# Optimization experiments

Measured on AMD Instinct MI355X. Metric: run time of the kernel, lower is better.

## Reference

```python
import jax, jax.numpy as jnp
import numpy as np

N = 50000      # nodes
D = 16         # fixed in-degree per node
E = N * D      # edges
C = 128        # in_channels == hidden_channels
H = 128        # hidden_channels
ED = 16        # edge_dim
OUT = 2        # out_channels


def setup_inputs() -> dict:
    key = jax.random.key(0)
    ks = jax.random.split(key, 16)
    s = 0.05
    x = jax.random.normal(ks[0], (N, C), jnp.float32)
    src = jax.random.randint(ks[1], (E,), 0, N)
    dst = jnp.repeat(jnp.arange(N), D)           # sorted by destination, degree D each
    edge_index = jnp.stack([src, dst]).astype(jnp.int32)
    edge_attr = jax.random.normal(ks[2], (E, ED), jnp.float32)
    # 3 SAGEConv layers, each: LSTM(C->C) aggregator + lin_l(C->H, bias) + lin_r(C->H, no bias)
    Wih = jax.random.normal(ks[3], (3, 4 * C, C), jnp.float32) * s
    Whh = jax.random.normal(ks[4], (3, 4 * C, C), jnp.float32) * s
    bih = jax.random.normal(ks[5], (3, 4 * C), jnp.float32) * s
    bhh = jax.random.normal(ks[6], (3, 4 * C), jnp.float32) * s
    lin_l_W = jax.random.normal(ks[7], (3, H, C), jnp.float32) * s
    lin_l_b = jax.random.normal(ks[8], (3, H), jnp.float32) * s
    lin_r_W = jax.random.normal(ks[9], (3, H, C), jnp.float32) * s
    # edge MLP: (2H+ED)->H->H//2->OUT
    W1 = jax.random.normal(ks[10], (H, 2 * H + ED), jnp.float32) * s
    b1 = jax.random.normal(ks[11], (H,), jnp.float32) * s
    W2 = jax.random.normal(ks[12], (H // 2, H), jnp.float32) * s
    b2 = jax.random.normal(ks[13], (H // 2,), jnp.float32) * s
    W3 = jax.random.normal(ks[14], (OUT, H // 2), jnp.float32) * s
    b3 = jax.random.normal(ks[15], (OUT,), jnp.float32) * s
    return dict(x=x, edge_index=edge_index, edge_attr=edge_attr,
                Wih=Wih, Whh=Whh, bih=bih, bhh=bhh,
                lin_l_W=lin_l_W, lin_l_b=lin_l_b, lin_r_W=lin_r_W,
                W1=W1, b1=b1, W2=W2, b2=b2, W3=W3, b3=b3)


def _lstm_last(seq, wih, whh, bi, bh):
    # seq: [N, D, C] -> last LSTM output [N, C] (torch gate order i,f,g,o)
    h0 = jnp.zeros((seq.shape[0], whh.shape[1]), seq.dtype)

    def step(carry, xt):
        h, c = carry
        gates = xt @ wih.T + bi + h @ whh.T + bh
        i, f, g, o = jnp.split(gates, 4, axis=-1)
        c = jax.nn.sigmoid(f) * c + jax.nn.sigmoid(i) * jnp.tanh(g)
        h = jax.nn.sigmoid(o) * jnp.tanh(c)
        return (h, c), None

    (h, _), _ = jax.lax.scan(step, (h0, h0), seq.transpose(1, 0, 2))
    return h


def _sage_lstm(x, src, wih, whh, bi, bh, wl, bl, wr):
    # fixed degree D, edges sorted by dst -> group-by-dst is a reshape
    seq = x[src].reshape(N, D, -1)           # [N, D, C] neighbor sequences
    agg = _lstm_last(seq, wih, whh, bi, bh)  # [N, C]
    return agg @ wl.T + bl + x @ wr.T        # lin_l(agg) + lin_r(x)


def reference(x, edge_index, edge_attr, Wih, Whh, bih, bhh,
              lin_l_W, lin_l_b, lin_r_W, W1, b1, W2, b2, W3, b3):
    src, dst = edge_index[0], edge_index[1]
    h = x
    for l in range(3):
        h = jax.nn.relu(_sage_lstm(h, src, Wih[l], Whh[l], bih[l], bhh[l],
                                   lin_l_W[l], lin_l_b[l], lin_r_W[l]))
    # gather-concat edge MLP (dropout is identity in eval)
    feat = jnp.concatenate([h[src], h[dst], edge_attr], axis=1)  # [E, 2H+ED]
    e = jax.nn.relu(feat @ W1.T + b1)
    e = jax.nn.relu(e @ W2.T + b2)
    return e @ W3.T + b3
```

## Files before the change

### kernel.cpp

```cpp
#include <hip/hip_runtime.h>
#include <hip/hip_bf16.h>

#define NN 50000
#define DEG 16

typedef __attribute__((ext_vector_type(8))) short bfrag;
typedef __attribute__((ext_vector_type(4))) float f32x4;

__device__ __forceinline__ float bf2f(unsigned int u){ return __uint_as_float(u<<16); }
__device__ __forceinline__ unsigned short f2bf(float x){
  unsigned int u = __float_as_uint(x);
  unsigned int r = (u + 0x7fffu + ((u>>16)&1u)) >> 16;
  return (unsigned short)r;
}
__device__ __forceinline__ float fast_rcp(float x){ return __builtin_amdgcn_rcpf(x); }
__device__ __forceinline__ float sigmoidf_(float x){ return fast_rcp(1.f + __expf(-x)); }
__device__ __forceinline__ float tanh_fast(float x){
  float e = __expf(-2.f*fabsf(x));
  float r = (1.f - e)*fast_rcp(1.f + e);
  return copysignf(r, x);
}

#define SWZ(row) (((((row) ^ ((row)>>3)) & 7)) << 4)
#define SW4(row) (((row) & 15) << 4)

#define GLDS16(g, l) __builtin_amdgcn_global_load_lds( \
    (const __attribute__((address_space(1))) unsigned int*)(g), \
    (__attribute__((address_space(3))) unsigned int*)(l), 16, 0, 0)

__global__ void k_cvt(const float* __restrict__ in, unsigned short* __restrict__ out, int n){
  int i = blockIdx.x*256 + threadIdx.x;
  if (i < n) out[i] = f2bf(in[i]);
}

__global__ void k_prep_all(const float* __restrict__ Wih, const float* __restrict__ Whh,
                           const float* __restrict__ bih, const float* __restrict__ bhh,
                           const float* __restrict__ WlL, const float* __restrict__ WrL,
                           const float* __restrict__ W1,  const float* __restrict__ W2,
                           const float* __restrict__ W3,
                           unsigned short* __restrict__ Wcat, float* __restrict__ bsum,
                           unsigned short* __restrict__ Wlb,  unsigned short* __restrict__ Wrb,
                           unsigned short* __restrict__ W1nb,
                           unsigned short* __restrict__ W1eh, unsigned short* __restrict__ W1el,
                           unsigned short* __restrict__ W2h,  unsigned short* __restrict__ W2l,
                           unsigned short* __restrict__ W3p)
{
  int i = blockIdx.x*256 + threadIdx.x;
  if (i < 393216){
    int l = i >> 17;
    int rem = i & 131071;
    int row = rem >> 8, col = rem & 255;
    float v = (col < 128) ? Wih[((size_t)l*512 + row)*128 + col]
                          : Whh[((size_t)l*512 + row)*128 + (col-128)];
    Wcat[i] = f2bf(v);
  } else if (i < 394752){
    int k = i - 393216;
    bsum[k] = bih[k] + bhh[k];
  } else if (i < 443904){
    int k = i - 394752;
    Wlb[k] = f2bf(WlL[k]);
  } else if (i < 493056){
    int k = i - 443904;
    Wrb[k] = f2bf(WrL[k]);
  } else if (i < 509440){
    int k = i - 493056; int r = k >> 7, c = k & 127;
    W1nb[k] = f2bf(W1[(size_t)r*272 + c]);
  } else if (i < 525824){
    int k = i - 509440; int r = k >> 7, c = k & 127;
    W1nb[16384 + k] = f2bf(W1[(size_t)r*272 + 128 + c]);
  } else if (i < 534016){
    int k = i - 525824;
    float v = W2[k];
    unsigned short hi = f2bf(v);
    W2h[k] = hi; W2l[k] = f2bf(v - bf2f(hi));
  } else if (i < 536064){
    int k = i - 534016; int j = k >> 4, kk = k & 15;
    float v = W1[(size_t)j*272 + 256 + kk];
    unsigned short hi = f2bf(v);
    W1eh[k] = hi; W1el[k] = f2bf(v - bf2f(hi));
  } else if (i < 537088){
    int k = i - 536064; int nr = k >> 6, c = k & 63;
    W3p[k] = f2bf(nr < 2 ? W3[nr*64 + c] : 0.f);
  }
}

__global__ __launch_bounds__(256,4) void k_bgemm(
    const unsigned short* __restrict__ Ab, const unsigned short* __restrict__ A2b,
    const unsigned short* __restrict__ Wb, const unsigned short* __restrict__ W2b,
    const float* __restrict__ bias, const float* __restrict__ bias2,
    float* __restrict__ outF, unsigned short* __restrict__ outB,
    int ostride, int dorelu, int n)
{
  const int t  = threadIdx.x;
  const int w  = t >> 6;
  const int l  = t & 63;
  const int ln = l & 15, q = l >> 4;
  const int n0 = blockIdx.x*64;
  const int j0 = blockIdx.y*128 + w*32;

  int nodeM[4];
#pragma unroll
  for (int mt=0;mt<4;mt++){ int nd = n0 + mt*16 + ln; nodeM[mt] = nd < n ? nd : n-1; }

  f32x4 acc[4][2];
#pragma unroll
  for (int mt=0;mt<4;mt++)
#pragma unroll
    for (int nt=0;nt<2;nt++) acc[mt][nt] = (f32x4){0.f,0.f,0.f,0.f};

  auto pass = [&](const unsigned short* __restrict__ Ap, const unsigned short* __restrict__ Wp){
#pragma unroll
    for (int ks=0;ks<4;ks++){
      bfrag Af[4], Bf[2];
#pragma unroll
      for (int mt=0;mt<4;mt++)
        Af[mt] = *(const bfrag*)(Ap + (size_t)nodeM[mt]*128 + ks*32 + q*8);
#pragma unroll
      for (int nt=0;nt<2;nt++)
        Bf[nt] = *(const bfrag*)(Wp + (size_t)(j0 + nt*16 + ln)*128 + ks*32 + q*8);
#pragma unroll
      for (int mt=0;mt<4;mt++)
#pragma unroll
        for (int nt=0;nt<2;nt++)
          acc[mt][nt] = __builtin_amdgcn_mfma_f32_16x16x32_bf16(Af[mt], Bf[nt], acc[mt][nt], 0,0,0);
    }
  };
  pass(Ab, Wb);
  if (A2b) pass(A2b, W2b);

#pragma unroll
  for (int nt=0;nt<2;nt++){
    int j = j0 + nt*16 + ln;
    float bv = bias ? bias[j] : 0.f;
    if (bias2) bv += bias2[j];
#pragma unroll
    for (int mt=0;mt<4;mt++)
#pragma unroll
      for (int r=0;r<4;r++){
        int row = n0 + mt*16 + q*4 + r;
        if (row < n){
          float v = acc[mt][nt][r] + bv;
          if (dorelu) v = fmaxf(v, 0.f);
          if (outF) outF[(size_t)row*ostride + j] = v;
          if (outB) outB[(size_t)row*ostride + j] = f2bf(v);
        }
      }
  }
}

__global__ __launch_bounds__(512,2) void k_lstm9(
    const unsigned short* __restrict__ xin,
    const int* __restrict__ src,
    const unsigned short* __restrict__ Wcat,
    const float* __restrict__ bsum,
    const unsigned short* __restrict__ Wlb,
    const unsigned short* __restrict__ Wrb,
    const float* __restrict__ bl,
    unsigned short* __restrict__ hout,
    int n)
{
  __shared__ unsigned short hs[64*128];
  __shared__ unsigned short xbuf[2][64*128];
  __shared__ int srcs[64*16];
  const int t  = threadIdx.x;
  const int w  = t >> 6;
  const int l  = t & 63;
  const int ln = l & 15;
  const int q  = l >> 4;
  const int n0 = blockIdx.x * 64;

  for (int i = t; i < 1024; i += 512){
    int nl = i >> 4, st = i & 15;
    srcs[i] = (n0+nl < n) ? src[(size_t)(n0+nl)*16 + st] : 0;
  }

  bfrag A[4][8];
#pragma unroll
  for (int T=0;T<4;T++)
#pragma unroll
    for (int ks=0;ks<8;ks++)
      A[T][ks] = *(const bfrag*)(Wcat + (size_t)(T*128 + w*16 + ln)*256 + ks*32 + q*8);

  f32x4 bsv[4];
#pragma unroll
  for (int T=0;T<4;T++)
    bsv[T] = *(const f32x4*)(bsum + T*128 + w*16 + q*4);

  float c[4][4];
#pragma unroll
  for (int nt=0;nt<4;nt++)
#pragma unroll
    for (int r=0;r<4;r++) c[nt][r]=0.f;

  __syncthreads();

  auto stageX = [&](int step, int buf){
#pragma unroll
    for (int j=0;j<2;j++){
      int row  = w*8 + j*4 + (l>>4);
      int node = srcs[row*16 + step];
      const char* gsrc = (const char*)xin + (size_t)node*256 + (((l&15)*16) ^ SW4(row));
      char* ldst = (char*)&xbuf[buf][0] + (w*8 + j*4)*256;
      GLDS16(gsrc, ldst);
    }
  };

  stageX(0, 0);
  asm volatile("s_waitcnt vmcnt(0)" ::: "memory");
  __syncthreads();

  for (int step=0; step<16; step++){
    const int cur = step & 1;
    if (step < 15) stageX(step+1, cur^1);

#pragma unroll
    for (int p=0;p<2;p++){
      f32x4 acc[4][2];
#pragma unroll
      for (int T=0;T<4;T++)
#pragma unroll
        for (int ntl=0;ntl<2;ntl++) acc[T][ntl] = (f32x4){0.f,0.f,0.f,0.f};

#pragma unroll
      for (int ntl=0; ntl<2; ntl++){
        int node = p*32 + ntl*16 + ln;
        int swz  = SW4(node);
#pragma unroll
        for (int ks=0;ks<4;ks++){
          bfrag Bk = *(const bfrag*)((const char*)&xbuf[cur][0] + node*256 +
                       ((ks*64 + q*16) ^ swz));
#pragma unroll
          for (int T=0;T<4;T++)
            acc[T][ntl] = __builtin_amdgcn_mfma_f32_16x16x32_bf16(A[T][ks], Bk, acc[T][ntl], 0,0,0);
        }
        if (step > 0){
#pragma unroll
          for (int ks=4;ks<8;ks++){
            bfrag Bk = *(const bfrag*)((const char*)hs + node*256 +
                         (((ks-4)*64 + q*16) ^ swz));
#pragma unroll
            for (int T=0;T<4;T++)
              acc[T][ntl] = __builtin_amdgcn_mfma_f32_16x16x32_bf16(A[T][ks], Bk, acc[T][ntl], 0,0,0);
          }
        }
      }

      if (p == 1){
        asm volatile("s_waitcnt vmcnt(0)" ::: "memory");
      }
      __syncthreads();

#pragma unroll
      for (int ntl=0; ntl<2; ntl++){
        int nt = p*2 + ntl;
        int node = p*32 + ntl*16 + ln;
        float h[4];
#pragma unroll
        for (int r=0;r<4;r++){
          float iv = acc[0][ntl][r] + bsv[0][r];
          float fv = acc[1][ntl][r] + bsv[1][r];
          float gg = acc[2][ntl][r] + bsv[2][r];
          float ov = acc[3][ntl][r] + bsv[3][r];
          float cn = sigmoidf_(fv)*c[nt][r] + sigmoidf_(iv)*tanh_fast(gg);
          c[nt][r] = cn;
          h[r] = sigmoidf_(ov)*tanh_fast(cn);
        }
        unsigned pk01, pk23;
        asm("v_cvt_pk_bf16_f32 %0, %1, %2" : "=v"(pk01) : "v"(h[0]), "v"(h[1]));
        asm("v_cvt_pk_bf16_f32 %0, %1, %2" : "=v"(pk23) : "v"(h[2]), "v"(h[3]));
        uint2 pv; pv.x = pk01; pv.y = pk23;
        *(uint2*)((char*)hs + node*256 + (((w*32 + q*8)) ^ SW4(node))) = pv;
      }
    }
  }

  __syncthreads();
  {
    bfrag Al[4], Ar[4];
#pragma unroll
    for (int ks=0;ks<4;ks++){
      Al[ks] = *(const bfrag*)(Wlb + (size_t)(w*16+ln)*128 + ks*32 + q*8);
      Ar[ks] = *(const bfrag*)(Wrb + (size_t)(w*16+ln)*128 + ks*32 + q*8);
    }
    f32x4 blv = *(const f32x4*)(bl + w*16 + q*4);
#pragma unroll
    for (int nt=0; nt<4; nt++){
      int node = nt*16 + ln;
      int gn = (n0+node < n) ? (n0+node) : (n-1);
      f32x4 acc = (f32x4){0.f,0.f,0.f,0.f};
#pragma unroll
      for (int ks=0;ks<4;ks++){
        bfrag Bh = *(const bfrag*)((const char*)hs + node*256 +
                     ((ks*64 + q*16) ^ SW4(node)));
        bfrag Bx = *(const bfrag*)(xin + (size_t)gn*128 + ks*32 + q*8);
        acc = __builtin_amdgcn_mfma_f32_16x16x32_bf16(Al[ks], Bh, acc, 0,0,0);
        acc = __builtin_amdgcn_mfma_f32_16x16x32_bf16(Ar[ks], Bx, acc, 0,0,0);
      }
      float v0 = fmaxf(acc[0]+blv[0], 0.f), v1 = fmaxf(acc[1]+blv[1], 0.f);
      float v2 = fmaxf(acc[2]+blv[2], 0.f), v3 = fmaxf(acc[3]+blv[3], 0.f);
      unsigned pk01, pk23;
      asm("v_cvt_pk_bf16_f32 %0, %1, %2" : "=v"(pk01) : "v"(v0), "v"(v1));
      asm("v_cvt_pk_bf16_f32 %0, %1, %2" : "=v"(pk23) : "v"(v2), "v"(v3));
      if (n0+node < n){
        uint2 pv; pv.x = pk01; pv.y = pk23;
        *(uint2*)(hout + (size_t)(n0+node)*128 + w*16 + q*4) = pv;
      }
    }
  }
}

__global__ __launch_bounds__(256,2) void k_edge4(
    const unsigned short* __restrict__ HsHd,
    const float* __restrict__ ea,
    const int* __restrict__ src,
    const unsigned short* __restrict__ W1eh, const unsigned short* __restrict__ W1el,
    const unsigned short* __restrict__ W2h,  const unsigned short* __restrict__ W2l,
    const unsigned short* __restrict__ W3p,
    const float* __restrict__ b1, const float* __restrict__ b2, const float* __restrict__ b3,
    float* __restrict__ out)
{
  __shared__ unsigned short out1h[64*128];
  __shared__ unsigned short out1l[64*128];
  __shared__ unsigned short e2h[64*64];
  __shared__ unsigned short e2l[64*64];
  __shared__ unsigned short ea2[64*56];

  const int t = threadIdx.x;
  const int w = t>>6, l = t&63, ln = l&15, q = l>>4;
  const int nblk = blockIdx.x;
  const size_t e0 = (size_t)nblk*64;

  int srcv[4];
#pragma unroll
  for (int r=0;r<4;r++) srcv[r] = src[e0 + w*16 + q*4 + r];

  unsigned short hsq[8][4];
#pragma unroll
  for (int nt=0;nt<8;nt++)
#pragma unroll
    for (int r=0;r<4;r++)
      hsq[nt][r] = HsHd[(size_t)srcv[r]*256 + nt*16 + ln];

  unsigned short hdq[8];
#pragma unroll
  for (int nt=0;nt<8;nt++)
    hdq[nt] = HsHd[((size_t)nblk*4 + w)*256 + 128 + nt*16 + ln];

  float b1v[8];
#pragma unroll
  for (int nt=0;nt<8;nt++) b1v[nt] = b1[nt*16 + ln];
  float b2v[4];
#pragma unroll
  for (int nt=0;nt<4;nt++) b2v[nt] = b2[nt*16 + ln];
  float b3v = (ln<2) ? b3[ln] : 0.f;

  bfrag w1h[8], w1l[8];
#pragma unroll
  for (int nt=0;nt<8;nt++){
    int j = nt*16 + ln;
    w1h[nt] = *(const bfrag*)(W1eh + (size_t)j*16 + (q&1)*8);
    w1l[nt] = *(const bfrag*)(W1el + (size_t)j*16 + (q&1)*8);
  }
  bfrag w3f[2];
#pragma unroll
  for (int ks=0;ks<2;ks++)
    w3f[ks] = *(const bfrag*)(W3p + (size_t)ln*64 + ks*32 + q*8);

  for (int i=t;i<1024;i+=256){
    int e=i>>4, k=i&15;
    float v = ea[(e0+e)*16 + k];
    unsigned short hi = f2bf(v);
    ea2[e*56 + k] = hi;
    ea2[e*56 + 16 + k] = f2bf(v - bf2f(hi));
  }
  __syncthreads();

  {
    bfrag Aea = *(const bfrag*)&ea2[(w*16+ln)*56 + q*8];
#pragma unroll
    for (int nt=0;nt<8;nt++){
      float hdv = bf2f((unsigned)hdq[nt]);
      f32x4 acc;
#pragma unroll
      for (int r=0;r<4;r++) acc[r] = b1v[nt] + hdv + bf2f((unsigned)hsq[nt][r]);
      acc = __builtin_amdgcn_mfma_f32_16x16x32_bf16(Aea, w1h[nt], acc, 0,0,0);
      acc = __builtin_amdgcn_mfma_f32_16x16x32_bf16(Aea, w1l[nt], acc, 0,0,0);
      int j = nt*16 + ln;
#pragma unroll
      for (int r=0;r<4;r++){
        int row = w*16 + q*4 + r;
        float v = fmaxf(acc[r], 0.f);
        unsigned short hi = f2bf(v);
        float lo = v - bf2f(hi);
        int byt = row*256 + ((j*2) ^ SWZ(row));
        *(unsigned short*)((char*)out1h + byt) = hi;
        *(unsigned short*)((char*)out1l + byt) = f2bf(lo);
      }
    }
  }
  __syncthreads();

  {
    f32x4 acc[4];
#pragma unroll
    for (int nt=0;nt<4;nt++) acc[nt] = (f32x4){b2v[nt],b2v[nt],b2v[nt],b2v[nt]};
    int arow = w*16 + ln;

    bfrag BhA[4], BlA[4], BhB[4], BlB[4];
#pragma unroll
    for (int nt=0;nt<4;nt++){
      int j = nt*16 + ln;
      BhA[nt] = *(const bfrag*)(W2h + (size_t)j*128 + q*8);
      BlA[nt] = *(const bfrag*)(W2l + (size_t)j*128 + q*8);
    }
#pragma unroll
    for (int ks=0;ks<4;ks++){
      if (ks < 3){
#pragma unroll
        for (int nt=0;nt<4;nt++){
          int j = nt*16 + ln;
          if ((ks&1)==0){
            BhB[nt] = *(const bfrag*)(W2h + (size_t)j*128 + (ks+1)*32 + q*8);
            BlB[nt] = *(const bfrag*)(W2l + (size_t)j*128 + (ks+1)*32 + q*8);
          } else {
            BhA[nt] = *(const bfrag*)(W2h + (size_t)j*128 + (ks+1)*32 + q*8);
            BlA[nt] = *(const bfrag*)(W2l + (size_t)j*128 + (ks+1)*32 + q*8);
          }
        }
      }
      int byt = arow*256 + ((ks*64 + q*16) ^ SWZ(arow));
      bfrag Ah = *(const bfrag*)((char*)out1h + byt);
      bfrag Al = *(const bfrag*)((char*)out1l + byt);
#pragma unroll
      for (int nt=0;nt<4;nt++){
        bfrag Bh = ((ks&1)==0) ? BhA[nt] : BhB[nt];
        bfrag Bl = ((ks&1)==0) ? BlA[nt] : BlB[nt];
        acc[nt] = __builtin_amdgcn_mfma_f32_16x16x32_bf16(Ah, Bh, acc[nt], 0,0,0);
        acc[nt] = __builtin_amdgcn_mfma_f32_16x16x32_bf16(Al, Bh, acc[nt], 0,0,0);
        acc[nt] = __builtin_amdgcn_mfma_f32_16x16x32_bf16(Ah, Bl, acc[nt], 0,0,0);
      }
    }
#pragma unroll
    for (int nt=0;nt<4;nt++)
#pragma unroll
      for (int r=0;r<4;r++){
        int row = w*16 + q*4 + r;
        int j = nt*16 + ln;
        float v = fmaxf(acc[nt][r], 0.f);
        unsigned short hi = f2bf(v);
        float lo = v - bf2f(hi);
        int byt = row*128 + ((j*2) ^ SWZ(row));
        *(unsigned short*)((char*)e2h + byt) = hi;
        *(unsigned short*)((char*)e2l + byt) = f2bf(lo);
      }
  }
  __syncthreads();

  {
    f32x4 acc = (f32x4){b3v,b3v,b3v,b3v};
    int arow = w*16 + ln;
#pragma unroll
    for (int ks=0;ks<2;ks++){
      int byt = arow*128 + ((ks*64 + q*16) ^ SWZ(arow));
      bfrag Ah = *(const bfrag*)((char*)e2h + byt);
      bfrag Al = *(const bfrag*)((char*)e2l + byt);
      acc = __builtin_amdgcn_mfma_f32_16x16x32_bf16(Ah, w3f[ks], acc, 0,0,0);
      acc = __builtin_amdgcn_mfma_f32_16x16x32_bf16(Al, w3f[ks], acc, 0,0,0);
    }
    if (ln < 2){
#pragma unroll
      for (int r=0;r<4;r++){
        int row = w*16 + q*4 + r;
        out[(e0 + row)*2 + ln] = acc[r];
      }
    }
  }
}

extern "C" void kernel_launch(void* const* d_in, const int* in_sizes, int n_in,
                              void* d_out, int out_size, void* d_ws, size_t ws_size,
                              hipStream_t stream) {
  const float* x    = (const float*)d_in[0];
  const int*   eidx = (const int*)  d_in[1];
  const float* eatt = (const float*)d_in[2];
  const float* Wih  = (const float*)d_in[3];
  const float* Whh  = (const float*)d_in[4];
  const float* bih  = (const float*)d_in[5];
  const float* bhh  = (const float*)d_in[6];
  const float* WlL  = (const float*)d_in[7];
  const float* blL  = (const float*)d_in[8];
  const float* WrL  = (const float*)d_in[9];
  const float* W1   = (const float*)d_in[10];
  const float* b1   = (const float*)d_in[11];
  const float* W2   = (const float*)d_in[12];
  const float* b2   = (const float*)d_in[13];
  const float* W3   = (const float*)d_in[14];
  const float* b3   = (const float*)d_in[15];
  const int*   src  = eidx;

  char* p = (char*)d_ws;
  unsigned short* HsHdB = (unsigned short*)p;
  p += (size_t)NN*512*2;
  unsigned short* xb   = (unsigned short*)p; p += (size_t)NN*128*2;
  unsigned short* hb1  = (unsigned short*)p; p += (size_t)NN*128*2;
  unsigned short* hb2  = (unsigned short*)p; p += (size_t)NN*128*2;
  unsigned short* Wcat = (unsigned short*)p; p += (size_t)3*512*256*2;
  float* bsum          = (float*)p;          p += (size_t)3*512*4;
  unsigned short* Wlb  = (unsigned short*)p; p += (size_t)3*128*128*2;
  unsigned short* Wrb  = (unsigned short*)p; p += (size_t)3*128*128*2;
  unsigned short* W1nb = (unsigned short*)p; p += (size_t)256*128*2;
  unsigned short* W1eh = (unsigned short*)p; p += 2048*2;
  unsigned short* W1el = (unsigned short*)p; p += 2048*2;
  unsigned short* W2h  = (unsigned short*)p; p += 8192*2;
  unsigned short* W2l  = (unsigned short*)p; p += 8192*2;
  unsigned short* W3p  = (unsigned short*)p; p += 1024*2;

  dim3 blk(256);
  const int nb = (NN + 63)/64;

  k_cvt<<<(NN*128+255)/256, blk, 0, stream>>>(x, xb, NN*128);
  k_prep_all<<<(537088+255)/256, blk, 0, stream>>>(Wih, Whh, bih, bhh, WlL, WrL, W1, W2, W3,
                                                   Wcat, bsum, Wlb, Wrb, W1nb,
                                                   W1eh, W1el, W2h, W2l, W3p);

  const unsigned short* hin = xb;
  unsigned short* houts[3] = {hb1, hb2, hb1};
  for (int l = 0; l < 3; l++){
    k_lstm9<<<dim3(nb),dim3(512),0,stream>>>(hin, src,
        Wcat + (size_t)l*512*256, bsum + (size_t)l*512,
        Wlb + (size_t)l*128*128, Wrb + (size_t)l*128*128, blL + (size_t)l*128,
        houts[l], NN);
    hin = houts[l];
  }
  k_bgemm<<<dim3(nb,2),blk,0,stream>>>(hin, nullptr, W1nb, nullptr,
                                       nullptr, nullptr, nullptr, HsHdB, 256, 0, NN);
  k_edge4<<<dim3(NN/4),blk,0,stream>>>(HsHdB, eatt, src, W1eh, W1el, W2h, W2l, W3p,
                                       b1, b2, b3, (float*)d_out);
}
```

Before: 1.382 ms.

## Split LSTM gate rows across 16 waves with packed weights and double-buffered h

The LSTM kernel moves from 8 to 16 waves per 64-node block. Each wave now holds 32 packed gate rows (two MFMA tiles) instead of 64, which halves the register-resident weight fragments. Gate values are exchanged between lane halves with xor-32 shuffles so that each lane can compute the i/f/g/o update for two hidden units. The weights and biases are repacked in the prep kernel to match. The hidden state is double-buffered so there is one barrier per timestep instead of two, at the cost of extra LDS, shuffle traffic and a tighter register budget at 1024 threads.

```diff
diff --git a/kernel.cpp b/kernel.cpp
--- a/kernel.cpp
+++ b/kernel.cpp
@@ -38,7 +38,7 @@
                            const float* __restrict__ WlL, const float* __restrict__ WrL,
                            const float* __restrict__ W1,  const float* __restrict__ W2,
                            const float* __restrict__ W3,
-                           unsigned short* __restrict__ Wcat, float* __restrict__ bsum,
+                           unsigned short* __restrict__ Wpck, float* __restrict__ bspck,
                            unsigned short* __restrict__ Wlb,  unsigned short* __restrict__ Wrb,
                            unsigned short* __restrict__ W1nb,
                            unsigned short* __restrict__ W1eh, unsigned short* __restrict__ W1el,
@@ -47,15 +47,22 @@
 {
   int i = blockIdx.x*256 + threadIdx.x;
   if (i < 393216){
-    int l = i >> 17;
+    int lidx = i >> 17;
     int rem = i & 131071;
-    int row = rem >> 8, col = rem & 255;
-    float v = (col < 128) ? Wih[((size_t)l*512 + row)*128 + col]
-                          : Whh[((size_t)l*512 + row)*128 + (col-128)];
-    Wcat[i] = f2bf(v);
+    int p = rem >> 8, col = rem & 255;
+    int wv = p >> 5, tl = (p >> 4) & 1, lr = p & 15;
+    int T = tl*2 + (lr >> 3), u = wv*8 + (lr & 7);
+    int R = T*128 + u;
+    float v = (col < 128) ? Wih[((size_t)lidx*512 + R)*128 + col]
+                          : Whh[((size_t)lidx*512 + R)*128 + (col-128)];
+    Wpck[i] = f2bf(v);
   } else if (i < 394752){
     int k = i - 393216;
-    bsum[k] = bih[k] + bhh[k];
+    int lidx = k >> 9; int p = k & 511;
+    int wv = p >> 5, tl = (p >> 4) & 1, lr = p & 15;
+    int T = tl*2 + (lr >> 3), u = wv*8 + (lr & 7);
+    int R = T*128 + u;
+    bspck[k] = bih[(size_t)lidx*512 + R] + bhh[(size_t)lidx*512 + R];
   } else if (i < 443904){
     int k = i - 394752;
     Wlb[k] = f2bf(WlL[k]);
@@ -148,20 +155,20 @@
   }
 }
 
-__global__ __launch_bounds__(512,2) void k_lstm9(
+__global__ __launch_bounds__(1024, 4) void k_lstm12(
     const unsigned short* __restrict__ xin,
     const int* __restrict__ src,
-    const unsigned short* __restrict__ Wcat,
-    const float* __restrict__ bsum,
+    const unsigned short* __restrict__ Wpck,
+    const float* __restrict__ bspck,
     const unsigned short* __restrict__ Wlb,
     const unsigned short* __restrict__ Wrb,
     const float* __restrict__ bl,
     unsigned short* __restrict__ hout,
     int n)
 {
-  __shared__ unsigned short hs[64*128];
+  __shared__ unsigned short hs[2][64*128];
   __shared__ unsigned short xbuf[2][64*128];
-  __shared__ int srcs[64*16];
+  __shared__ int srcs[1024];
   const int t  = threadIdx.x;
   const int w  = t >> 6;
   const int l  = t & 63;
@@ -169,128 +176,134 @@
   const int q  = l >> 4;
   const int n0 = blockIdx.x * 64;
 
-  for (int i = t; i < 1024; i += 512){
-    int nl = i >> 4, st = i & 15;
-    srcs[i] = (n0+nl < n) ? src[(size_t)(n0+nl)*16 + st] : 0;
-  }
-
-  bfrag A[4][8];
-#pragma unroll
-  for (int T=0;T<4;T++)
-#pragma unroll
-    for (int ks=0;ks<8;ks++)
-      A[T][ks] = *(const bfrag*)(Wcat + (size_t)(T*128 + w*16 + ln)*256 + ks*32 + q*8);
-
-  f32x4 bsv[4];
-#pragma unroll
-  for (int T=0;T<4;T++)
-    bsv[T] = *(const f32x4*)(bsum + T*128 + w*16 + q*4);
-
-  float c[4][4];
-#pragma unroll
-  for (int nt=0;nt<4;nt++)
-#pragma unroll
-    for (int r=0;r<4;r++) c[nt][r]=0.f;
+  { int nl = t >> 4, st = t & 15;
+    srcs[t] = (n0+nl < n) ? src[(size_t)(n0+nl)*16 + st] : 0; }
+
+  bfrag A[2][8];
+#pragma unroll
+  for (int tl=0; tl<2; tl++)
+#pragma unroll
+    for (int ks=0; ks<8; ks++)
+      A[tl][ks] = *(const bfrag*)(Wpck + (size_t)(w*32 + tl*16 + ln)*256 + ks*32 + q*8);
+
+  f32x4 bs0 = *(const f32x4*)(bspck + w*32 + q*4);
+  f32x4 bs1 = *(const f32x4*)(bspck + w*32 + 16 + q*4);
+  f32x4 ob0, ob1;
+#pragma unroll
+  for (int i=0;i<4;i++){
+    ob0[i] = __shfl_xor(bs0[i], 32, 64);
+    ob1[i] = __shfl_xor(bs1[i], 32, 64);
+  }
+  const bool lo = (q < 2);
+  float bI[2], bF[2], bG[2], bO[2];
+#pragma unroll
+  for (int rr=0; rr<2; rr++){
+    float a0 = lo ? bs0[rr] : bs0[2+rr];
+    float p0 = lo ? ob0[rr] : ob0[2+rr];
+    float a1 = lo ? bs1[rr] : bs1[2+rr];
+    float p1 = lo ? ob1[rr] : ob1[2+rr];
+    bI[rr] = lo ? a0 : p0;
+    bF[rr] = lo ? p0 : a0;
+    bG[rr] = lo ? a1 : p1;
+    bO[rr] = lo ? p1 : a1;
+  }
+
+  float c[4][2];
+#pragma unroll
+  for (int nt=0;nt<4;nt++){ c[nt][0]=0.f; c[nt][1]=0.f; }
 
   __syncthreads();
 
   auto stageX = [&](int step, int buf){
-#pragma unroll
-    for (int j=0;j<2;j++){
-      int row  = w*8 + j*4 + (l>>4);
-      int node = srcs[row*16 + step];
-      const char* gsrc = (const char*)xin + (size_t)node*256 + (((l&15)*16) ^ SW4(row));
-      char* ldst = (char*)&xbuf[buf][0] + (w*8 + j*4)*256;
-      GLDS16(gsrc, ldst);
-    }
+    int row  = w*4 + (l>>4);
+    int node = srcs[row*16 + step];
+    const char* gsrc = (const char*)xin + (size_t)node*256 + (((l&15)*16) ^ SW4(row));
+    char* ldst = (char*)&xbuf[buf][0] + (w*4)*256;
+    GLDS16(gsrc, ldst);
   };
 
   stageX(0, 0);
   asm volatile("s_waitcnt vmcnt(0)" ::: "memory");
   __syncthreads();
 
+  const int hwoff = w*16 + (q&1)*8 + (q>>1)*4;
+
   for (int step=0; step<16; step++){
-    const int cur = step & 1;
-    if (step < 15) stageX(step+1, cur^1);
-
-#pragma unroll
-    for (int p=0;p<2;p++){
-      f32x4 acc[4][2];
-#pragma unroll
-      for (int T=0;T<4;T++)
-#pragma unroll
-        for (int ntl=0;ntl<2;ntl++) acc[T][ntl] = (f32x4){0.f,0.f,0.f,0.f};
-
-#pragma unroll
-      for (int ntl=0; ntl<2; ntl++){
-        int node = p*32 + ntl*16 + ln;
-        int swz  = SW4(node);
-#pragma unroll
-        for (int ks=0;ks<4;ks++){
-          bfrag Bk = *(const bfrag*)((const char*)&xbuf[cur][0] + node*256 +
-                       ((ks*64 + q*16) ^ swz));
-#pragma unroll
-          for (int T=0;T<4;T++)
-            acc[T][ntl] = __builtin_amdgcn_mfma_f32_16x16x32_bf16(A[T][ks], Bk, acc[T][ntl], 0,0,0);
+    const int xcur = step & 1;
+    const int hrb  = step & 1;
+    const int hwb  = hrb ^ 1;
+    if (step < 15) stageX(step+1, xcur^1);
+
+#pragma unroll
+    for (int nt=0; nt<4; nt++){
+      int node = nt*16 + ln;
+      int swz  = SW4(node);
+      f32x4 acc0 = (f32x4){0.f,0.f,0.f,0.f};
+      f32x4 acc1 = (f32x4){0.f,0.f,0.f,0.f};
+#pragma unroll
+      for (int ks=0;ks<4;ks++){
+        bfrag Bk = *(const bfrag*)((const char*)&xbuf[xcur][0] + node*256 +
+                     ((ks*64 + q*16) ^ swz));
+        acc0 = __builtin_amdgcn_mfma_f32_16x16x32_bf16(A[0][ks], Bk, acc0, 0,0,0);
+        acc1 = __builtin_amdgcn_mfma_f32_16x16x32_bf16(A[1][ks], Bk, acc1, 0,0,0);
+      }
+      if (step > 0){
+#pragma unroll
+        for (int ks=4;ks<8;ks++){
+          bfrag Bk = *(const bfrag*)((const char*)&hs[hrb][0] + node*256 +
+                       (((ks-4)*64 + q*16) ^ swz));
+          acc0 = __builtin_amdgcn_mfma_f32_16x16x32_bf16(A[0][ks], Bk, acc0, 0,0,0);
+          acc1 = __builtin_amdgcn_mfma_f32_16x16x32_bf16(A[1][ks], Bk, acc1, 0,0,0);
         }
-        if (step > 0){
-#pragma unroll
-          for (int ks=4;ks<8;ks++){
-            bfrag Bk = *(const bfrag*)((const char*)hs + node*256 +
-                         (((ks-4)*64 + q*16) ^ swz));
-#pragma unroll
-            for (int T=0;T<4;T++)
-              acc[T][ntl] = __builtin_amdgcn_mfma_f32_16x16x32_bf16(A[T][ks], Bk, acc[T][ntl], 0,0,0);
-          }
-        }
-      }
-
-      if (p == 1){
-        asm volatile("s_waitcnt vmcnt(0)" ::: "memory");
-      }
-      __syncthreads();
-
-#pragma unroll
-      for (int ntl=0; ntl<2; ntl++){
-        int nt = p*2 + ntl;
-        int node = p*32 + ntl*16 + ln;
-        float h[4];
-#pragma unroll
-        for (int r=0;r<4;r++){
-          float iv = acc[0][ntl][r] + bsv[0][r];
-          float fv = acc[1][ntl][r] + bsv[1][r];
-          float gg = acc[2][ntl][r] + bsv[2][r];
-          float ov = acc[3][ntl][r] + bsv[3][r];
-          float cn = sigmoidf_(fv)*c[nt][r] + sigmoidf_(iv)*tanh_fast(gg);
-          c[nt][r] = cn;
-          h[r] = sigmoidf_(ov)*tanh_fast(cn);
-        }
-        unsigned pk01, pk23;
-        asm("v_cvt_pk_bf16_f32 %0, %1, %2" : "=v"(pk01) : "v"(h[0]), "v"(h[1]));
-        asm("v_cvt_pk_bf16_f32 %0, %1, %2" : "=v"(pk23) : "v"(h[2]), "v"(h[3]));
-        uint2 pv; pv.x = pk01; pv.y = pk23;
-        *(uint2*)((char*)hs + node*256 + (((w*32 + q*8)) ^ SW4(node))) = pv;
-      }
-    }
-  }
-
-  __syncthreads();
+      }
+      f32x4 o0, o1;
+#pragma unroll
+      for (int i=0;i<4;i++){
+        o0[i] = __shfl_xor(acc0[i], 32, 64);
+        o1[i] = __shfl_xor(acc1[i], 32, 64);
+      }
+      float h2[2];
+#pragma unroll
+      for (int rr=0; rr<2; rr++){
+        float a0 = lo ? acc0[rr] : acc0[2+rr];
+        float p0 = lo ? o0[rr]   : o0[2+rr];
+        float a1 = lo ? acc1[rr] : acc1[2+rr];
+        float p1 = lo ? o1[rr]   : o1[2+rr];
+        float iv = (lo ? a0 : p0) + bI[rr];
+        float fv = (lo ? p0 : a0) + bF[rr];
+        float gg = (lo ? a1 : p1) + bG[rr];
+        float ov = (lo ? p1 : a1) + bO[rr];
+        float cn = sigmoidf_(fv)*c[nt][rr] + sigmoidf_(iv)*tanh_fast(gg);
+        c[nt][rr] = cn;
+        h2[rr] = sigmoidf_(ov)*tanh_fast(cn);
+      }
+      unsigned pk;
+      asm("v_cvt_pk_bf16_f32 %0, %1, %2" : "=v"(pk) : "v"(h2[0]), "v"(h2[1]));
+      *(unsigned*)((char*)&hs[hwb][0] + node*256 + (hwoff ^ swz)) = pk;
+    }
+    asm volatile("s_waitcnt vmcnt(0)" ::: "memory");
+    __syncthreads();
+  }
+
   {
+    const int jw  = w & 7;
+    const int ntb = (w >> 3) * 2;
     bfrag Al[4], Ar[4];
 #pragma unroll
     for (int ks=0;ks<4;ks++){
-      Al[ks] = *(const bfrag*)(Wlb + (size_t)(w*16+ln)*128 + ks*32 + q*8);
-      Ar[ks] = *(const bfrag*)(Wrb + (size_t)(w*16+ln)*128 + ks*32 + q*8);
-    }
-    f32x4 blv = *(const f32x4*)(bl + w*16 + q*4);
-#pragma unroll
-    for (int nt=0; nt<4; nt++){
+      Al[ks] = *(const bfrag*)(Wlb + (size_t)(jw*16+ln)*128 + ks*32 + q*8);
+      Ar[ks] = *(const bfrag*)(Wrb + (size_t)(jw*16+ln)*128 + ks*32 + q*8);
+    }
+    f32x4 blv = *(const f32x4*)(bl + jw*16 + q*4);
+#pragma unroll
+    for (int nn=0; nn<2; nn++){
+      int nt = ntb + nn;
       int node = nt*16 + ln;
       int gn = (n0+node < n) ? (n0+node) : (n-1);
       f32x4 acc = (f32x4){0.f,0.f,0.f,0.f};
 #pragma unroll
       for (int ks=0;ks<4;ks++){
-        bfrag Bh = *(const bfrag*)((const char*)hs + node*256 +
+        bfrag Bh = *(const bfrag*)((const char*)&hs[0][0] + node*256 +
                      ((ks*64 + q*16) ^ SW4(node)));
         bfrag Bx = *(const bfrag*)(xin + (size_t)gn*128 + ks*32 + q*8);
         acc = __builtin_amdgcn_mfma_f32_16x16x32_bf16(Al[ks], Bh, acc, 0,0,0);
@@ -303,7 +316,7 @@
       asm("v_cvt_pk_bf16_f32 %0, %1, %2" : "=v"(pk23) : "v"(v2), "v"(v3));
       if (n0+node < n){
         uint2 pv; pv.x = pk01; pv.y = pk23;
-        *(uint2*)(hout + (size_t)(n0+node)*128 + w*16 + q*4) = pv;
+        *(uint2*)(hout + (size_t)(n0+node)*128 + jw*16 + q*4) = pv;
       }
     }
   }
@@ -391,10 +404,10 @@
         int row = w*16 + q*4 + r;
         float v = fmaxf(acc[r], 0.f);
         unsigned short hi = f2bf(v);
-        float lo = v - bf2f(hi);
+        float lov = v - bf2f(hi);
         int byt = row*256 + ((j*2) ^ SWZ(row));
         *(unsigned short*)((char*)out1h + byt) = hi;
-        *(unsigned short*)((char*)out1l + byt) = f2bf(lo);
+        *(unsigned short*)((char*)out1l + byt) = f2bf(lov);
       }
     }
   }
@@ -448,10 +461,10 @@
         int j = nt*16 + ln;
         float v = fmaxf(acc[nt][r], 0.f);
         unsigned short hi = f2bf(v);
-        float lo = v - bf2f(hi);
+        float lov = v - bf2f(hi);
         int byt = row*128 + ((j*2) ^ SWZ(row));
         *(unsigned short*)((char*)e2h + byt) = hi;
-        *(unsigned short*)((char*)e2l + byt) = f2bf(lo);
+        *(unsigned short*)((char*)e2l + byt) = f2bf(lov);
       }
   }
   __syncthreads();
@@ -504,8 +517,8 @@
   unsigned short* xb   = (unsigned short*)p; p += (size_t)NN*128*2;
   unsigned short* hb1  = (unsigned short*)p; p += (size_t)NN*128*2;
   unsigned short* hb2  = (unsigned short*)p; p += (size_t)NN*128*2;
-  unsigned short* Wcat = (unsigned short*)p; p += (size_t)3*512*256*2;
-  float* bsum          = (float*)p;          p += (size_t)3*512*4;
+  unsigned short* Wpck = (unsigned short*)p; p += (size_t)3*512*256*2;
+  float* bspck         = (float*)p;          p += (size_t)3*512*4;
   unsigned short* Wlb  = (unsigned short*)p; p += (size_t)3*128*128*2;
   unsigned short* Wrb  = (unsigned short*)p; p += (size_t)3*128*128*2;
   unsigned short* W1nb = (unsigned short*)p; p += (size_t)256*128*2;
@@ -520,14 +533,14 @@
 
   k_cvt<<<(NN*128+255)/256, blk, 0, stream>>>(x, xb, NN*128);
   k_prep_all<<<(537088+255)/256, blk, 0, stream>>>(Wih, Whh, bih, bhh, WlL, WrL, W1, W2, W3,
-                                                   Wcat, bsum, Wlb, Wrb, W1nb,
+                                                   Wpck, bspck, Wlb, Wrb, W1nb,
                                                    W1eh, W1el, W2h, W2l, W3p);
 
   const unsigned short* hin = xb;
   unsigned short* houts[3] = {hb1, hb2, hb1};
   for (int l = 0; l < 3; l++){
-    k_lstm9<<<dim3(nb),dim3(512),0,stream>>>(hin, src,
-        Wcat + (size_t)l*512*256, bsum + (size_t)l*512,
+    k_lstm12<<<dim3(nb),dim3(1024),0,stream>>>(hin, src,
+        Wpck + (size_t)l*512*256, bspck + (size_t)l*512,
         Wlb + (size_t)l*128*128, Wrb + (size_t)l*128*128, blL + (size_t)l*128,
         houts[l], NN);
     hin = houts[l];
```

Result: slower. 1.431 ms (+3.6%).
